# Optimization experiments

Measured on AMD Instinct MI355X. Metric: run time of the kernel, lower is better.

The kernel has to match this reference:

```python
import jax, jax.numpy as jnp
import numpy as np

UNITS = 512
D_Q = 1024
D_V = 1024


def setup_inputs() -> dict:
    key = jax.random.key(0)
    ks = jax.random.split(key, 12)
    B, L = 32, 2048
    inp = {
        "query": jax.random.normal(ks[0], (B, D_Q), jnp.float32),
        "values": jax.random.normal(ks[1], (B, L, D_V), jnp.float32),
        "mask": jnp.zeros((B, L, 1), jnp.float32),
        "previous_scores": jax.random.uniform(ks[2], (B, L, 1), jnp.float32),
        "timestep": 3,
        # Dense params (glorot-ish scale)
        "Wh": jax.random.normal(ks[3], (D_Q, UNITS), jnp.float32) / np.sqrt(D_Q),
        "bh": jnp.zeros((UNITS,), jnp.float32),
        "Wv": jax.random.normal(ks[4], (D_V, UNITS), jnp.float32) / np.sqrt(D_V),
        "bv": jnp.zeros((UNITS,), jnp.float32),
        "Wp": jax.random.normal(ks[5], (3, UNITS), jnp.float32) / np.sqrt(3.0),
        "bp": jnp.zeros((UNITS,), jnp.float32),
        "Wm": jax.random.normal(ks[6], (5, UNITS), jnp.float32) / np.sqrt(5.0),
        "bm": jnp.zeros((UNITS,), jnp.float32),
        "vw": jax.random.normal(ks[7], (UNITS, 1), jnp.float32) / np.sqrt(UNITS),
        "vb": jnp.zeros((1,), jnp.float32),
    }
    return inp


def reference(query, values, mask, previous_scores, timestep,
              Wh, bh, Wv, bv, Wp, bp, Wm, bm, vw, vb):
    B, L, _ = mask.shape
    # input_lengths: 1 + count of mask==0 along seq, tiled across L  -> [B, L, 1]
    input_len = 1.0 + jnp.sum((mask == 0).astype(jnp.float32), axis=1)  # [B, 1]
    input_len = jnp.broadcast_to(input_len, (B, L))[..., None]          # [B, L, 1]
    # positional features: [1+timestep, 2+pos, input_len], logged -> [B, L, 3]
    pos2 = jnp.stack([jnp.full((L,), 1.0 + timestep, jnp.float32),
                      2.0 + jnp.arange(L, dtype=jnp.float32)], axis=-1)  # [L, 2]
    pos2 = jnp.broadcast_to(pos2[None], (B, L, 2))
    positional = jnp.log(jnp.concatenate([pos2, input_len], axis=-1))    # [B, L, 3]
    # markov: sliding window of width 5 over zero-padded previous scores -> [B, L, 5]
    padded = jnp.pad(previous_scores[:, :, 0], ((0, 0), (2, 2)))         # [B, L+4]
    widx = jnp.arange(L)[:, None] + jnp.arange(5)[None, :]               # [L, 5]
    markov = padded[:, widx]                                             # [B, L, 5]
    # additive attention score
    summand = (jnp.einsum('bq,qu->bu', query, Wh) + bh)[:, None, :]      # [B, 1, U]
    summand = summand + (jnp.einsum('blv,vu->blu', values, Wv) + bv)
    summand = summand + (jnp.einsum('blp,pu->blu', positional, Wp) + bp)
    summand = summand + (jnp.einsum('blm,mu->blu', markov, Wm) + bm)
    score = jnp.einsum('blu,uo->blo', jnp.tanh(summand), vw) + vb        # [B, L, 1]
    score = score + mask * (-1e9)
    attention_weights = jax.nn.softmax(score, axis=1)                    # [B, L, 1]
    context_vector = jnp.sum(attention_weights * values, axis=1)         # [B, D_V]
    return (context_vector, attention_weights)
```

## Files before the change

### kernel.cpp

```cpp
#include <hip/hip_runtime.h>
#include <hip/hip_bf16.h>
#include <math.h>

#define NB 32
#define LL 2048
#define DV 1024
#define NU 512
#define NM (NB * LL)

typedef __attribute__((ext_vector_type(8))) short short8;
typedef __attribute__((ext_vector_type(4))) float f32x4;

#define GLL16(g, l)                                                            \
  __builtin_amdgcn_global_load_lds(                                            \
      (const __attribute__((address_space(1))) void*)(g),                      \
      (__attribute__((address_space(3))) void*)(l), 16, 0, 0)

__device__ __forceinline__ float fast_tanh(float x) {
  x = fminf(fmaxf(x, -15.f), 15.f);
  float e = __expf(2.f * x);
  return (e - 1.f) / (e + 1.f);
}

__global__ __launch_bounds__(256) void masksum_kernel(
    const float* __restrict__ mask, float* __restrict__ loglen) {
  int b = blockIdx.x, tid = threadIdx.x;
  int lane = tid & 63, wid = tid >> 6;
  float c = 0.f;
#pragma unroll
  for (int j = 0; j < 8; j++)
    c += (mask[(size_t)b * LL + j * 256 + tid] == 0.f) ? 1.f : 0.f;
#pragma unroll
  for (int o = 32; o >= 1; o >>= 1) c += __shfl_xor(c, o, 64);
  __shared__ float red[4];
  if (lane == 0) red[wid] = c;
  __syncthreads();
  if (tid == 0) loglen[b] = logf(1.f + red[0] + red[1] + red[2] + red[3]);
}

__global__ __launch_bounds__(256) void wvpack_kernel(
    const float* __restrict__ Wv, __hip_bfloat16* __restrict__ wvpk) {
  int idx = blockIdx.x * 256 + threadIdx.x;
  int c = idx & 3;
  int n = (idx >> 2) & 255;
  int kt = (idx >> 10) & 31;
  int nt = idx >> 15;
  int q = c ^ ((n >> 1) & 3);
  int u = nt * 256 + n;
  int k0 = kt * 32 + q * 8;
  union {
    __hip_bfloat162 h2[4];
    int4 v;
  } pk;
#pragma unroll
  for (int e = 0; e < 4; e++) {
    float a = Wv[(size_t)(k0 + 2 * e) * NU + u];
    float b = Wv[(size_t)(k0 + 2 * e + 1) * NU + u];
    pk.h2[e] = __float22bfloat162_rn(make_float2(a, b));
  }
  ((int4*)wvpk)[idx] = pk.v;
}

__global__ __launch_bounds__(512) void h_kernel(
    const float* __restrict__ q, const float* __restrict__ Wh,
    const float* __restrict__ bh, const float* __restrict__ bv,
    const float* __restrict__ bp, const float* __restrict__ bm,
    const float* __restrict__ Wp, const int* __restrict__ ts,
    const float* __restrict__ loglen, float* __restrict__ h) {
  int b = blockIdx.x, ks = blockIdx.y;
  int u = threadIdx.x;
  __shared__ float qs[128];
  if (u < 128) qs[u] = q[b * 1024 + ks * 128 + u];
  __syncthreads();
  float acc = 0.f;
#pragma unroll 8
  for (int k = 0; k < 128; k++)
    acc += qs[k] * Wh[(size_t)(ks * 128 + k) * NU + u];
  if (ks == 0) {
    float lt = logf(1.0f + (float)ts[0]);
    acc += bh[u] + bv[u] + bp[u] + bm[u] + lt * Wp[u] + loglen[b] * Wp[2 * NU + u];
  }
  atomicAdd(&h[b * NU + u], acc);
}

__global__ __launch_bounds__(256, 2) void score_kernel(
    const float* __restrict__ values, const __hip_bfloat16* __restrict__ wvpk,
    const float* __restrict__ h, const float* __restrict__ Wp,
    const float* __restrict__ Wm, const float* __restrict__ vw,
    const float* __restrict__ prev, float* __restrict__ partial) {
  int lin = blockIdx.x;
  int group = lin >> 4, sub = lin & 15;
  int ntile = sub >> 3;
  int mtile = group * 8 + (sub & 7);
  int tid = threadIdx.x;
  int lane = tid & 63, wid = tid >> 6;
  int wr = wid >> 1, wc = wid & 1;
  int col = lane & 15, quad = lane >> 4;
  int b = mtile >> 4;
  int l0 = (mtile & 15) << 7;
  int rowbase = mtile << 7;

  __shared__ __align__(16) char AsB[8192];
  __shared__ __align__(16) char BsB[16384];
  __shared__ float hL[256], wp1L[256], vwL[256], wmL[5][256];
  __shared__ float loglS[128], prevs[132], scoreAcc[128];

  {
    int u = ntile * 256 + tid;
    hL[tid] = h[b * NU + u];
    wp1L[tid] = Wp[NU + u];
    vwL[tid] = vw[u];
#pragma unroll
    for (int j = 0; j < 5; j++) wmL[j][tid] = Wm[j * NU + u];
  }
  if (tid < 128) {
    loglS[tid] = __logf(2.0f + (float)(l0 + tid));
    scoreAcc[tid] = 0.f;
  }
  if (tid < 132) {
    int li = l0 - 2 + tid;
    prevs[tid] = (li >= 0 && li < LL) ? prev[(size_t)b * LL + li] : 0.f;
  }

  f32x4 acc[4][8];
  f32x4 zero4 = {0.f, 0.f, 0.f, 0.f};
#pragma unroll
  for (int i = 0; i < 4; i++)
#pragma unroll
    for (int j = 0; j < 8; j++) acc[i][j] = zero4;

  int row = tid >> 1, h0 = tid & 1;
  const float* abase = values + (size_t)(rowbase + row) * DV + h0 * 16;
  int s_sw = (row >> 1) & 3;
  char* adst0 = AsB + row * 64 + (((h0 * 2) ^ s_sw) * 16);
  char* adst1 = AsB + row * 64 + (((h0 * 2 + 1) ^ s_sw) * 16);
  const char* bbase = (const char*)wvpk + (size_t)ntile * 32 * 16384;
  int boff = tid * 16;

  float4 preA[2][4];
#pragma unroll
  for (int d = 0; d < 2; d++) {
    const float4* p = (const float4*)(abase + d * 32);
#pragma unroll
    for (int j = 0; j < 4; j++) preA[d][j] = p[j];
  }

#define KSTEP(KT, PBUF)                                                        \
  {                                                                            \
    __syncthreads();                       \
    const char* bsrc = bbase + (size_t)(KT) * 16384;                           \
    GLL16(bsrc + boff, BsB + boff);                                            \
    GLL16(bsrc + boff + 4096, BsB + boff + 4096);                              \
    GLL16(bsrc + boff + 8192, BsB + boff + 8192);                              \
    GLL16(bsrc + boff + 12288, BsB + boff + 12288);                            \
    float4 f0 = preA[PBUF][0], f1 = preA[PBUF][1];                             \
    float4 f2 = preA[PBUF][2], f3 = preA[PBUF][3];                             \
    union {                                                                    \
      __hip_bfloat162 h2[8];                                                   \
      int4 qq[2];                                                              \
    } pk;                                                                      \
    pk.h2[0] = __float22bfloat162_rn(make_float2(f0.x, f0.y));                 \
    pk.h2[1] = __float22bfloat162_rn(make_float2(f0.z, f0.w));                 \
    pk.h2[2] = __float22bfloat162_rn(make_float2(f1.x, f1.y));                 \
    pk.h2[3] = __float22bfloat162_rn(make_float2(f1.z, f1.w));                 \
    pk.h2[4] = __float22bfloat162_rn(make_float2(f2.x, f2.y));                 \
    pk.h2[5] = __float22bfloat162_rn(make_float2(f2.z, f2.w));                 \
    pk.h2[6] = __float22bfloat162_rn(make_float2(f3.x, f3.y));                 \
    pk.h2[7] = __float22bfloat162_rn(make_float2(f3.z, f3.w));                 \
    *(int4*)adst0 = pk.qq[0];                                                  \
    *(int4*)adst1 = pk.qq[1];                                                  \
    __syncthreads();               \
    if ((KT) < 30) {      \
      const float4* nx = (const float4*)(abase + ((KT) + 2) * 32);             \
      preA[PBUF][0] = nx[0];                                                   \
      preA[PBUF][1] = nx[1];                                                   \
      preA[PBUF][2] = nx[2];                                                   \
      preA[PBUF][3] = nx[3];                                                   \
    }                                                                          \
    short8 aF[4];                                                              \
    _Pragma("unroll") for (int t = 0; t < 4; t++) {                            \
      int m = wr * 64 + t * 16 + col;                                          \
      aF[t] = *(const short8*)(AsB + m * 64 + ((quad ^ ((m >> 1) & 3)) * 16)); \
    }                                                                          \
    _Pragma("unroll") for (int tc = 0; tc < 8; tc++) {                         \
      int n = wc * 128 + tc * 16 + col;                                        \
      short8 bF =                                                              \
          *(const short8*)(BsB + n * 64 + ((quad ^ ((n >> 1) & 3)) * 16));     \
      _Pragma("unroll") for (int tr = 0; tr < 4; tr++) acc[tr][tc] =           \
          __builtin_amdgcn_mfma_f32_16x16x32_bf16(aF[tr], bF, acc[tr][tc], 0,  \
                                                  0, 0);                       \
    }                                                                          \
  }

  for (int kto = 0; kto < 16; kto++) {
    KSTEP(2 * kto, 0);
    KSTEP(2 * kto + 1, 1);
  }
#undef KSTEP

  int rb = wr * 64;
#pragma unroll
  for (int tr = 0; tr < 4; tr++) {
    float ps[4] = {0.f, 0.f, 0.f, 0.f};
#pragma unroll
    for (int tc = 0; tc < 8; tc++) {
      int uc = wc * 128 + tc * 16 + col;
      float hh = hL[uc], wp1 = wp1L[uc], vv = vwL[uc];
      float m0 = wmL[0][uc], m1 = wmL[1][uc], m2 = wmL[2][uc],
            m3 = wmL[3][uc], m4 = wmL[4][uc];
      int r0 = rb + tr * 16 + quad * 4;
#pragma unroll
      for (int i = 0; i < 4; i++) {
        int r = r0 + i;
        float e = hh + loglS[r] * wp1 + prevs[r] * m0 + prevs[r + 1] * m1 +
                  prevs[r + 2] * m2 + prevs[r + 3] * m3 + prevs[r + 4] * m4;
        float sv = acc[tr][tc][i] + e;
        ps[i] += fast_tanh(sv) * vv;
      }
    }
#pragma unroll
    for (int i = 0; i < 4; i++) {
      float v = ps[i];
      v += __shfl_xor(v, 1, 64);
      v += __shfl_xor(v, 2, 64);
      v += __shfl_xor(v, 4, 64);
      v += __shfl_xor(v, 8, 64);
      if (col == 0) atomicAdd(&scoreAcc[rb + tr * 16 + quad * 4 + i], v);
    }
  }
  __syncthreads();
  if (tid < 128)
    partial[(size_t)ntile * NM + rowbase + tid] = scoreAcc[tid];
}

__global__ __launch_bounds__(256) void softmax_kernel(
    const float* __restrict__ partial, const float* __restrict__ mask,
    float* __restrict__ aw) {
  int b = blockIdx.x, tid = threadIdx.x;
  int lane = tid & 63, wid = tid >> 6;
  __shared__ float redmax[4], redsum[4];
  float sc[8];
  float mx = -3.0e38f;
#pragma unroll
  for (int j = 0; j < 8; j++) {
    size_t base = (size_t)b * LL + j * 256 + tid;
    float s = partial[base] + partial[(size_t)NM + base];
    s += mask[base] * -1.0e9f;
    sc[j] = s;
    mx = fmaxf(mx, s);
  }
#pragma unroll
  for (int o = 32; o >= 1; o >>= 1) mx = fmaxf(mx, __shfl_xor(mx, o, 64));
  if (lane == 0) redmax[wid] = mx;
  __syncthreads();
  mx = fmaxf(fmaxf(redmax[0], redmax[1]), fmaxf(redmax[2], redmax[3]));
  float sum = 0.f;
#pragma unroll
  for (int j = 0; j < 8; j++) {
    float e = __expf(sc[j] - mx);
    sc[j] = e;
    sum += e;
  }
#pragma unroll
  for (int o = 32; o >= 1; o >>= 1) sum += __shfl_xor(sum, o, 64);
  if (lane == 0) redsum[wid] = sum;
  __syncthreads();
  sum = redsum[0] + redsum[1] + redsum[2] + redsum[3];
  float inv = 1.0f / sum;
#pragma unroll
  for (int j = 0; j < 8; j++)
    aw[(size_t)b * LL + j * 256 + tid] = sc[j] * inv;
}

__global__ __launch_bounds__(256) void ctx_kernel(
    const float* __restrict__ values, const float* __restrict__ aw,
    float* __restrict__ out) {
  int b = blockIdx.x, lq = blockIdx.y, tid = threadIdx.x;
  const float4* vrow =
      (const float4*)(values + ((size_t)b * LL + lq * 64) * DV) + tid;
  const float* awb = aw + (size_t)b * LL + lq * 64;
  float4 acc = make_float4(0.f, 0.f, 0.f, 0.f);
#pragma unroll 8
  for (int l = 0; l < 64; l++) {
    float w = awb[l];
    float4 v = vrow[(size_t)l * 256];
    acc.x += w * v.x;
    acc.y += w * v.y;
    acc.z += w * v.z;
    acc.w += w * v.w;
  }
  float* o = out + (size_t)b * DV + tid * 4;
  atomicAdd(o + 0, acc.x);
  atomicAdd(o + 1, acc.y);
  atomicAdd(o + 2, acc.z);
  atomicAdd(o + 3, acc.w);
}

extern "C" void kernel_launch(void* const* d_in, const int* in_sizes, int n_in,
                              void* d_out, int out_size, void* d_ws,
                              size_t ws_size, hipStream_t stream) {
  const float* query = (const float*)d_in[0];
  const float* values = (const float*)d_in[1];
  const float* mask = (const float*)d_in[2];
  const float* prev = (const float*)d_in[3];
  const int* ts = (const int*)d_in[4];
  const float* Wh = (const float*)d_in[5];
  const float* bh = (const float*)d_in[6];
  const float* Wv = (const float*)d_in[7];
  const float* bv = (const float*)d_in[8];
  const float* Wp = (const float*)d_in[9];
  const float* bp = (const float*)d_in[10];
  const float* Wm = (const float*)d_in[11];
  const float* bm = (const float*)d_in[12];
  const float* vw = (const float*)d_in[13];

  float* out = (float*)d_out;
  float* ws = (float*)d_ws;
  float* loglen = ws;
  float* h = ws + 1024;
  float* partial = ws + 32768;
  __hip_bfloat16* wvpk =
      (__hip_bfloat16*)((char*)d_ws + (size_t)163840 * 4);
  float* aw = out + 32768;

  hipMemsetAsync(d_out, 0, 32768 * sizeof(float), stream);
  hipMemsetAsync((char*)d_ws + 4096, 0, 16384 * sizeof(float), stream);
  masksum_kernel<<<NB, 256, 0, stream>>>(mask, loglen);
  wvpack_kernel<<<256, 256, 0, stream>>>(Wv, wvpk);
  h_kernel<<<dim3(NB, 8), 512, 0, stream>>>(query, Wh, bh, bv, bp, bm, Wp, ts,
                                            loglen, h);
  score_kernel<<<1024, 256, 0, stream>>>(values, wvpk, h, Wp, Wm, vw, prev,
                                         partial);
  softmax_kernel<<<NB, 256, 0, stream>>>(partial, mask, aw);
  ctx_kernel<<<dim3(NB, 32), 256, 0, stream>>>(values, aw, out);
}
```

Measured before the change: 513.3 us.

## Double-buffer LDS tiles to overlap next-stage loads with MFMA compute

Splits the A and B shared-memory tiles into two buffers so that stage k+1 is loaded (weights via global_load_lds, values converted to bf16) while stage k's MFMAs run. This leaves one barrier per k-step instead of two and hides load latency behind compute. In exchange LDS use doubles to about 48KB of tile buffers, which may limit the two-blocks-per-CU occupancy, and the prefetch indices now follow a more complex schedule.

New measurement: 513.1 us. No clear change (-0.0%).

```diff
diff --git a/kernel.cpp b/kernel.cpp
--- a/kernel.cpp
+++ b/kernel.cpp
@@ -100,8 +100,8 @@
   int l0 = (mtile & 15) << 7;
   int rowbase = mtile << 7;
 
-  __shared__ __align__(16) char AsB[8192];
-  __shared__ __align__(16) char BsB[16384];
+  __shared__ __align__(16) char AsB[2][8192];
+  __shared__ __align__(16) char BsB[2][16384];
   __shared__ float hL[256], wp1L[256], vwL[256], wmL[5][256];
   __shared__ float loglS[128], prevs[132], scoreAcc[128];
 
@@ -132,70 +132,105 @@
   int row = tid >> 1, h0 = tid & 1;
   const float* abase = values + (size_t)(rowbase + row) * DV + h0 * 16;
   int s_sw = (row >> 1) & 3;
-  char* adst0 = AsB + row * 64 + (((h0 * 2) ^ s_sw) * 16);
-  char* adst1 = AsB + row * 64 + (((h0 * 2 + 1) ^ s_sw) * 16);
+  int aoff0 = row * 64 + (((h0 * 2) ^ s_sw) * 16);
+  int aoff1 = row * 64 + (((h0 * 2 + 1) ^ s_sw) * 16);
   const char* bbase = (const char*)wvpk + (size_t)ntile * 32 * 16384;
   int boff = tid * 16;
 
   float4 preA[2][4];
-#pragma unroll
-  for (int d = 0; d < 2; d++) {
-    const float4* p = (const float4*)(abase + d * 32);
-#pragma unroll
-    for (int j = 0; j < 4; j++) preA[d][j] = p[j];
-  }
-
-#define KSTEP(KT, PBUF)                                                        \
+
+  {
+#pragma unroll
+    for (int d = 0; d < 2; d++) {
+      const float4* p = (const float4*)(abase + d * 32);
+#pragma unroll
+      for (int j = 0; j < 4; j++) preA[d][j] = p[j];
+    }
+    GLL16(bbase + boff, BsB[0] + boff);
+    GLL16(bbase + boff + 4096, BsB[0] + boff + 4096);
+    GLL16(bbase + boff + 8192, BsB[0] + boff + 8192);
+    GLL16(bbase + boff + 12288, BsB[0] + boff + 12288);
+    float4 f0 = preA[0][0], f1 = preA[0][1];
+    float4 f2 = preA[0][2], f3 = preA[0][3];
+    union {
+      __hip_bfloat162 h2[8];
+      int4 qq[2];
+    } pk;
+    pk.h2[0] = __float22bfloat162_rn(make_float2(f0.x, f0.y));
+    pk.h2[1] = __float22bfloat162_rn(make_float2(f0.z, f0.w));
+    pk.h2[2] = __float22bfloat162_rn(make_float2(f1.x, f1.y));
+    pk.h2[3] = __float22bfloat162_rn(make_float2(f1.z, f1.w));
+    pk.h2[4] = __float22bfloat162_rn(make_float2(f2.x, f2.y));
+    pk.h2[5] = __float22bfloat162_rn(make_float2(f2.z, f2.w));
+    pk.h2[6] = __float22bfloat162_rn(make_float2(f3.x, f3.y));
+    pk.h2[7] = __float22bfloat162_rn(make_float2(f3.z, f3.w));
+    *(int4*)(AsB[0] + aoff0) = pk.qq[0];
+    *(int4*)(AsB[0] + aoff1) = pk.qq[1];
+    const float4* nx = (const float4*)(abase + 2 * 32);
+    preA[0][0] = nx[0];
+    preA[0][1] = nx[1];
+    preA[0][2] = nx[2];
+    preA[0][3] = nx[3];
+    __syncthreads();
+  }
+
+#define KSTEP(KT, CBUF, OSLOT, DO_STAGE, DO_RELOAD)                            \
   {                                                                            \
-    __syncthreads();                       \
-    const char* bsrc = bbase + (size_t)(KT) * 16384;                           \
-    GLL16(bsrc + boff, BsB + boff);                                            \
-    GLL16(bsrc + boff + 4096, BsB + boff + 4096);                              \
-    GLL16(bsrc + boff + 8192, BsB + boff + 8192);                              \
-    GLL16(bsrc + boff + 12288, BsB + boff + 12288);                            \
-    float4 f0 = preA[PBUF][0], f1 = preA[PBUF][1];                             \
-    float4 f2 = preA[PBUF][2], f3 = preA[PBUF][3];                             \
-    union {                                                                    \
-      __hip_bfloat162 h2[8];                                                   \
-      int4 qq[2];                                                              \
-    } pk;                                                                      \
-    pk.h2[0] = __float22bfloat162_rn(make_float2(f0.x, f0.y));                 \
-    pk.h2[1] = __float22bfloat162_rn(make_float2(f0.z, f0.w));                 \
-    pk.h2[2] = __float22bfloat162_rn(make_float2(f1.x, f1.y));                 \
-    pk.h2[3] = __float22bfloat162_rn(make_float2(f1.z, f1.w));                 \
-    pk.h2[4] = __float22bfloat162_rn(make_float2(f2.x, f2.y));                 \
-    pk.h2[5] = __float22bfloat162_rn(make_float2(f2.z, f2.w));                 \
-    pk.h2[6] = __float22bfloat162_rn(make_float2(f3.x, f3.y));                 \
-    pk.h2[7] = __float22bfloat162_rn(make_float2(f3.z, f3.w));                 \
-    *(int4*)adst0 = pk.qq[0];                                                  \
-    *(int4*)adst1 = pk.qq[1];                                                  \
-    __syncthreads();               \
-    if ((KT) < 30) {      \
-      const float4* nx = (const float4*)(abase + ((KT) + 2) * 32);             \
-      preA[PBUF][0] = nx[0];                                                   \
-      preA[PBUF][1] = nx[1];                                                   \
-      preA[PBUF][2] = nx[2];                                                   \
-      preA[PBUF][3] = nx[3];                                                   \
+    if (DO_STAGE) {                                                            \
+      const char* bsrc = bbase + (size_t)((KT) + 1) * 16384;                   \
+      GLL16(bsrc + boff, BsB[(CBUF) ^ 1] + boff);                              \
+      GLL16(bsrc + boff + 4096, BsB[(CBUF) ^ 1] + boff + 4096);                \
+      GLL16(bsrc + boff + 8192, BsB[(CBUF) ^ 1] + boff + 8192);                \
+      GLL16(bsrc + boff + 12288, BsB[(CBUF) ^ 1] + boff + 12288);              \
+      float4 f0 = preA[OSLOT][0], f1 = preA[OSLOT][1];                         \
+      float4 f2 = preA[OSLOT][2], f3 = preA[OSLOT][3];                         \
+      union {                                                                  \
+        __hip_bfloat162 h2[8];                                                 \
+        int4 qq[2];                                                            \
+      } pk;                                                                    \
+      pk.h2[0] = __float22bfloat162_rn(make_float2(f0.x, f0.y));               \
+      pk.h2[1] = __float22bfloat162_rn(make_float2(f0.z, f0.w));               \
+      pk.h2[2] = __float22bfloat162_rn(make_float2(f1.x, f1.y));               \
+      pk.h2[3] = __float22bfloat162_rn(make_float2(f1.z, f1.w));               \
+      pk.h2[4] = __float22bfloat162_rn(make_float2(f2.x, f2.y));               \
+      pk.h2[5] = __float22bfloat162_rn(make_float2(f2.z, f2.w));               \
+      pk.h2[6] = __float22bfloat162_rn(make_float2(f3.x, f3.y));               \
+      pk.h2[7] = __float22bfloat162_rn(make_float2(f3.z, f3.w));               \
+      *(int4*)(AsB[(CBUF) ^ 1] + aoff0) = pk.qq[0];                            \
+      *(int4*)(AsB[(CBUF) ^ 1] + aoff1) = pk.qq[1];                            \
+      if (DO_RELOAD) {                                                         \
+        const float4* nx = (const float4*)(abase + ((KT) + 3) * 32);           \
+        preA[OSLOT][0] = nx[0];                                                \
+        preA[OSLOT][1] = nx[1];                                                \
+        preA[OSLOT][2] = nx[2];                                                \
+        preA[OSLOT][3] = nx[3];                                                \
+      }                                                                        \
     }                                                                          \
     short8 aF[4];                                                              \
     _Pragma("unroll") for (int t = 0; t < 4; t++) {                            \
       int m = wr * 64 + t * 16 + col;                                          \
-      aF[t] = *(const short8*)(AsB + m * 64 + ((quad ^ ((m >> 1) & 3)) * 16)); \
+      aF[t] = *(const short8*)(AsB[CBUF] + m * 64 +                            \
+                               ((quad ^ ((m >> 1) & 3)) * 16));                \
     }                                                                          \
     _Pragma("unroll") for (int tc = 0; tc < 8; tc++) {                         \
       int n = wc * 128 + tc * 16 + col;                                        \
       short8 bF =                                                              \
-          *(const short8*)(BsB + n * 64 + ((quad ^ ((n >> 1) & 3)) * 16));     \
+          *(const short8*)(BsB[CBUF] + n * 64 + ((quad ^ ((n >> 1) & 3)) * 16)); \
       _Pragma("unroll") for (int tr = 0; tr < 4; tr++) acc[tr][tc] =           \
           __builtin_amdgcn_mfma_f32_16x16x32_bf16(aF[tr], bF, acc[tr][tc], 0,  \
                                                   0, 0);                       \
     }                                                                          \
-  }
-
-  for (int kto = 0; kto < 16; kto++) {
-    KSTEP(2 * kto, 0);
-    KSTEP(2 * kto + 1, 1);
-  }
+    __syncthreads();                                                           \
+  }
+
+  for (int kto = 0; kto < 14; kto++) {
+    KSTEP(2 * kto, 0, 1, 1, 1);
+    KSTEP(2 * kto + 1, 1, 0, 1, 1);
+  }
+  KSTEP(28, 0, 1, 1, 1);
+  KSTEP(29, 1, 0, 1, 0);
+  KSTEP(30, 0, 1, 1, 0);
+  KSTEP(31, 1, 0, 0, 0);
 #undef KSTEP
 
   int rb = wr * 64;
```
